# Kernel optimization log

Hardware: AMD Instinct MI355X
Metric: run time of the kernel (lower is better)

Reference implementation:

```python
import jax, jax.numpy as jnp
import numpy as np
import math

B, T, C = 2, 2048, 1024
H, D = 16, 64
GAMMA = 8

def setup_inputs() -> dict:
    key = jax.random.key(0)
    ks = jax.random.split(key, 6)
    s = 1.0 / math.sqrt(C)  # keep pre-softmax scores well-scaled
    return {
        "x": jax.random.normal(ks[0], (B, T, C), jnp.float32),
        "Wq": jax.random.normal(ks[1], (C, 2 * C), jnp.float32) * s,
        "Wk": jax.random.normal(ks[2], (C, 2 * C), jnp.float32) * s,
        "Wv": jax.random.normal(ks[3], (C, C), jnp.float32) * s,
        "Wo": jax.random.normal(ks[4], (C, C), jnp.float32) * s,
        "theta_offset": jax.random.normal(ks[5], (H,), jnp.float32) * 0.1,
    }

def _heads(t):  # (B,T,C) -> (B,H,T,D)
    return t.reshape(B, T, H, D).transpose(0, 2, 1, 3)

def reference(x, Wq, Wk, Wv, Wo, theta_offset):
    scale = 1.0 / math.sqrt(D)
    q_raw = x @ Wq            # (B,T,2C)
    k_raw = x @ Wk
    v = _heads(x @ Wv)        # (B,H,T,D)
    q_amp, q_phase = _heads(q_raw[..., :C]), _heads(q_raw[..., C:])
    k_amp, k_phase = _heads(k_raw[..., :C]), _heads(k_raw[..., C:])
    q_amp = jax.nn.softplus(q_amp)
    k_amp = jax.nn.softplus(k_amp)
    # sum_d a_q a_k cos(p_q - p_k) = (a_q cos p_q)(a_k cos p_k) + (a_q sin p_q)(a_k sin p_k)
    qc, qs = q_amp * jnp.cos(q_phase), q_amp * jnp.sin(q_phase)
    kc, ks_ = k_amp * jnp.cos(k_phase), k_amp * jnp.sin(k_phase)
    scores = (jnp.einsum('bhqd,bhkd->bhqk', qc, kc)
              + jnp.einsum('bhqd,bhkd->bhqk', qs, ks_)) * scale
    if T > GAMMA:  # theta gating
        cid = jnp.arange(T, dtype=jnp.float32) / GAMMA
        cycle_dist = cid[None, :] - cid[:, None]          # (T,T): cid[j]-cid[i]
        gate = jnp.cos(theta_offset[:, None, None] * cycle_dist[None])  # (H,T,T)
        scores = scores * gate[None]
    causal = jnp.tril(jnp.ones((T, T), dtype=bool))
    scores = jnp.where(causal[None, None], scores, -jnp.inf)
    attn = jax.nn.softmax(scores, axis=-1)
    out = jnp.einsum('bhqk,bhkd->bhqd', attn, v)
    out = out.transpose(0, 2, 1, 3).reshape(B, T, C)
    return out @ Wo
```

## Files before the change

### kernel.cpp

```cpp
#include <hip/hip_runtime.h>
#include <cmath>

namespace {

constexpr int B_ = 2, T_ = 2048, C_ = 1024, H_ = 16;
constexpr float GAMMA_INV = 0.125f;
constexpr float SCALE = 0.125f;
constexpr float LOG2E = 1.4426950408889634f;
constexpr float THR2 = 11.5415603f;

typedef __attribute__((ext_vector_type(8))) short bf16x8;
typedef __attribute__((ext_vector_type(4))) float f32x4;
typedef unsigned short ushort_t;

__device__ __forceinline__ ushort_t f2bf(float x) {
  union { float f; unsigned int u; } v; v.f = x;
  unsigned int r = (v.u + 0x7fffu + ((v.u >> 16) & 1u)) >> 16;
  return (ushort_t)r;
}

__device__ __forceinline__ unsigned pk_bf16(float a, float b) {
  unsigned r;
  asm("v_cvt_pk_bf16_f32 %0, %1, %2" : "=v"(r) : "v"(a), "v"(b));
  return r;
}

__device__ __forceinline__ float fexp2(float x) {
  return __builtin_amdgcn_exp2f(x);
}

__device__ __forceinline__ f32x4 mfma16(bf16x8 a, bf16x8 b, f32x4 c) {
  return __builtin_amdgcn_mfma_f32_16x16x32_bf16(a, b, c, 0, 0, 0);
}

__device__ __forceinline__ void gld_lds16(const ushort_t* g, ushort_t* l) {
  __builtin_amdgcn_global_load_lds(
      (const __attribute__((address_space(1))) unsigned int*)g,
      (__attribute__((address_space(3))) unsigned int*)l, 16, 0, 0);
}

constexpr int GBM = 128, GBN = 128, GBK = 64;

#define GEMM_CORE(A_, Bt_, K_)                                                  \
  __shared__ ushort_t As[GBM][GBK];                                             \
  __shared__ ushort_t Bs[GBN][GBK];                                             \
  const int tid = threadIdx.x;                                                  \
  const int wv = tid >> 6;                                                      \
  const int ln = tid & 63;                                                      \
  const int lr = ln & 15, hi = ln >> 4;                                         \
  const int wr = wv >> 1, wc = wv & 1;                                          \
  const int srow8 = tid >> 3;                                                   \
  const int ssw = ((tid & 7) ^ (srow8 & 7)) * 8;                                \
  const int kxg = (lr & 7) << 3;                                                \
  f32x4 acc[4][4];                                                              \
  _Pragma("unroll")                                                             \
  for (int m = 0; m < 4; ++m)                                                   \
    _Pragma("unroll")                                                           \
    for (int n = 0; n < 4; ++n)                                                 \
      _Pragma("unroll")                                                         \
      for (int r = 0; r < 4; ++r) acc[m][n][r] = 0.0f;                          \
  for (int k0 = 0; k0 < K_; k0 += GBK) {                                        \
    _Pragma("unroll")                                                           \
    for (int p = 0; p < 4; ++p) {                                               \
      gld_lds16(A_ + (size_t)(m0 + p * 32 + srow8) * K_ + k0 + ssw,             \
                &As[0][0] + p * 2048 + wv * 512);                               \
      gld_lds16(Bt_ + (size_t)(n0 + p * 32 + srow8) * K_ + k0 + ssw,            \
                &Bs[0][0] + p * 2048 + wv * 512);                               \
    }                                                                           \
    __syncthreads();                                                            \
    _Pragma("unroll")                                                           \
    for (int ks = 0; ks < 2; ++ks) {                                            \
      bf16x8 af[4], bfr[4];                                                     \
      _Pragma("unroll")                                                         \
      for (int m = 0; m < 4; ++m)                                               \
        af[m] = *(const bf16x8*)&As[wr * 64 + m * 16 + lr]                      \
                                  [(ks * 32 + hi * 8) ^ kxg];                   \
      _Pragma("unroll")                                                         \
      for (int n = 0; n < 4; ++n)                                               \
        bfr[n] = *(const bf16x8*)&Bs[wc * 64 + n * 16 + lr]                     \
                                   [(ks * 32 + hi * 8) ^ kxg];                  \
      _Pragma("unroll")                                                         \
      for (int m = 0; m < 4; ++m)                                               \
        _Pragma("unroll")                                                       \
        for (int n = 0; n < 4; ++n)                                             \
          acc[m][n] = mfma16(af[m], bfr[n], acc[m][n]);                         \
    }                                                                           \
    __syncthreads();                                                            \
  }

__global__ __launch_bounds__(256) void gemm_f32out(const ushort_t* __restrict__ A,
                                                   const ushort_t* __restrict__ Bt,
                                                   float* __restrict__ Cm,
                                                   int N, int K) {
  const int m0 = blockIdx.y * GBM, n0 = blockIdx.x * GBN;
  GEMM_CORE(A, Bt, K)
  #pragma unroll
  for (int m = 0; m < 4; ++m) {
    #pragma unroll
    for (int r = 0; r < 4; ++r) {
      const int row = m0 + wr * 64 + m * 16 + hi * 4 + r;
      float* Crow = Cm + (size_t)row * N + n0 + wc * 64;
      #pragma unroll
      for (int n = 0; n < 4; ++n)
        Crow[n * 16 + lr] = acc[m][n][r];
    }
  }
}

__global__ __launch_bounds__(256) void gemm_qkv(const ushort_t* __restrict__ A,
                                                const ushort_t* __restrict__ Bt,
                                                ushort_t* __restrict__ Qb,
                                                ushort_t* __restrict__ Kb,
                                                ushort_t* __restrict__ Vb,
                                                int K) {
  const int m0 = blockIdx.y * GBM, n0 = blockIdx.x * GBN;
  GEMM_CORE(A, Bt, K)
  if (n0 < 4096) {
    const int isK = (n0 >> 11) & 1;
    ushort_t* Dst = isK ? Kb : Qb;
    const int odd = lr & 1;
    #pragma unroll
    for (int m = 0; m < 4; ++m) {
      #pragma unroll
      for (int r = 0; r < 4; ++r) {
        const int row = m0 + wr * 64 + m * 16 + hi * 4 + r;
        #pragma unroll
        for (int n = 0; n < 4; ++n) {
          const int nn = n0 + wc * 64 + n * 16 + lr;
          float x = acc[m][n][r];
          float y = __shfl_xor(x, 1);
          float amp = odd ? y : x;
          float ph  = odd ? x : y;
          float sp = (amp > 20.f) ? amp : __logf(1.0f + __expf(amp));
          float val = sp * (odd ? __sinf(ph) : __cosf(ph));
          const int cc = (nn & 2047) >> 1;
          const int h = cc >> 6, d = cc & 63;
          const int t = row & (T_ - 1), b = row >> 11;
          Dst[(((size_t)(b * H_ + h) * T_) + t) * 128 + d + (odd ? 64 : 0)] = f2bf(val);
        }
      }
    }
  } else {
    const int v0 = n0 - 4096;
    #pragma unroll
    for (int m = 0; m < 4; ++m) {
      #pragma unroll
      for (int r = 0; r < 4; ++r) {
        const int row = m0 + wr * 64 + m * 16 + hi * 4 + r;
        ushort_t* Crow = Vb + (size_t)row * 1024 + v0 + wc * 64;
        #pragma unroll
        for (int n = 0; n < 4; ++n)
          Crow[n * 16 + lr] = f2bf(acc[m][n][r]);
      }
    }
  }
}

__global__ __launch_bounds__(256) void prep(const float* __restrict__ x,
                                            const float* __restrict__ Wq,
                                            const float* __restrict__ Wk,
                                            const float* __restrict__ Wv,
                                            const float* __restrict__ Wo,
                                            ushort_t* __restrict__ xb,
                                            ushort_t* __restrict__ Wqkt,
                                            ushort_t* __restrict__ Wvt,
                                            ushort_t* __restrict__ Wot) {
  __shared__ float tf[32][33];
  const int id = blockIdx.x;
  const int i = threadIdx.x;
  if (id < 4096) {
    const int e = (id * 256 + i) * 4;
    float4 a = *(const float4*)&x[e];
    uint2 p;
    p.x = (unsigned)f2bf(a.x) | ((unsigned)f2bf(a.y) << 16);
    p.y = (unsigned)f2bf(a.z) | ((unsigned)f2bf(a.w) << 16);
    *(uint2*)&xb[e] = p;
  } else if (id < 8192) {
    const int id2 = id - 4096;
    const int k0 = (id2 & 31) * 32, n0 = (id2 >> 5) * 32;
    const float* src = (n0 < 2048) ? Wq : Wk;
    const int c0 = (n0 & 2047) >> 1;
    {
      const int r = i >> 3, c4 = (i & 7) * 4;
      const int scol = (c4 < 16) ? (c0 + c4) : (1024 + c0 + c4 - 16);
      float4 v = *(const float4*)&src[(size_t)(k0 + r) * 2048 + scol];
      tf[r][c4 + 0] = v.x; tf[r][c4 + 1] = v.y; tf[r][c4 + 2] = v.z; tf[r][c4 + 3] = v.w;
    }
    __syncthreads();
    {
      const int orow = i >> 3, k4 = (i & 7) * 4;
      const int sel = (orow >> 1) + ((orow & 1) ? 16 : 0);
      uint2 p;
      p.x = (unsigned)f2bf(tf[k4 + 0][sel]) | ((unsigned)f2bf(tf[k4 + 1][sel]) << 16);
      p.y = (unsigned)f2bf(tf[k4 + 2][sel]) | ((unsigned)f2bf(tf[k4 + 3][sel]) << 16);
      *(uint2*)&Wqkt[(size_t)(n0 + orow) * 1024 + k0 + k4] = p;
    }
  } else {
    const int id3 = (id < 9216) ? (id - 8192) : (id - 9216);
    const float* W = (id < 9216) ? Wv : Wo;
    ushort_t* Wt = (id < 9216) ? Wvt : Wot;
    const int k0 = (id3 >> 5) * 32, n0 = (id3 & 31) * 32;
    {
      const int r = i >> 3, c4 = (i & 7) * 4;
      float4 v = *(const float4*)&W[(size_t)(k0 + r) * 1024 + n0 + c4];
      tf[r][c4 + 0] = v.x; tf[r][c4 + 1] = v.y; tf[r][c4 + 2] = v.z; tf[r][c4 + 3] = v.w;
    }
    __syncthreads();
    {
      const int r = i >> 3, c4 = (i & 7) * 4;
      uint2 p;
      p.x = (unsigned)f2bf(tf[c4 + 0][r]) | ((unsigned)f2bf(tf[c4 + 1][r]) << 16);
      p.y = (unsigned)f2bf(tf[c4 + 2][r]) | ((unsigned)f2bf(tf[c4 + 3][r]) << 16);
      *(uint2*)&Wt[(size_t)(n0 + r) * 1024 + k0 + c4] = p;
    }
  }
}

__global__ __launch_bounds__(256) void v_transpose(const ushort_t* __restrict__ V,
                                                   ushort_t* __restrict__ VT) {
  const int bh = blockIdx.y;
  const int b = bh >> 4, h = bh & 15;
  const int t0 = blockIdx.x * 32;
  __shared__ ushort_t lds[32][72];
  const int i = threadIdx.x;
  {
    int r = i >> 3, d0 = (i & 7) * 8;
    const ushort_t* src = V + ((size_t)(b * T_) + t0 + r) * C_ + h * 64 + d0;
    uint4 v = *(const uint4*)src;
    *(uint4*)&lds[r][d0] = v;
  }
  __syncthreads();
  {
    int d = i >> 2, tq = (i & 3) * 8;
    ushort_t tmp[8];
    #pragma unroll
    for (int j = 0; j < 8; ++j) tmp[j] = lds[tq + j][d];
    ulonglong2 pk;
    pk.x = (unsigned long long)tmp[0] | ((unsigned long long)tmp[1] << 16) |
           ((unsigned long long)tmp[2] << 32) | ((unsigned long long)tmp[3] << 48);
    pk.y = (unsigned long long)tmp[4] | ((unsigned long long)tmp[5] << 16) |
           ((unsigned long long)tmp[6] << 32) | ((unsigned long long)tmp[7] << 48);
    *(ulonglong2*)(VT + ((size_t)bh * 64 + d) * T_ + t0 + tq) = pk;
  }
}

__global__ __launch_bounds__(256) void attn_split(const ushort_t* __restrict__ Q,
                                                  const ushort_t* __restrict__ K,
                                                  const ushort_t* __restrict__ VT,
                                                  const float* __restrict__ theta,
                                                  unsigned* __restrict__ Op,
                                                  float* __restrict__ mpart,
                                                  float* __restrict__ lpart) {
  const int id = blockIdx.x;
  const int xcd = id & 7, sub = id >> 3;
  const int bhl = sub / 40;
  const int u = 39 - (sub - bhl * 40);
  int qt, s, ns;
  if (u < 4)       { qt = u;                 s = 0;             ns = 1; }
  else if (u < 12) { qt = 4 + ((u - 4) >> 1);  s = (u - 4) & 1;   ns = 2; }
  else if (u < 24) { qt = 8 + (u - 12) / 3;    s = (u - 12) % 3;  ns = 3; }
  else             { qt = 12 + ((u - 24) >> 2); s = (u - 24) & 3; ns = 4; }
  const int nktf = 2 * qt + 2;
  const int t0 = (s * nktf) / ns;
  const int t1 = ((s + 1) * nktf) / ns;
  const int bh = xcd * 4 + bhl;
  const int p = bh * 40 + u;
  unsigned* Op_my = Op + (size_t)p * 4096;

  const int h = bh & 15;
  const int tid = threadIdx.x;
  const int wid = tid >> 6, lane = tid & 63;
  const int q_base = qt * 128 + wid * 32;
  const int lr = lane & 15, lg = lane >> 4;
  const int kx = (lr & 7) << 4;

  __shared__ alignas(16) ushort_t Ksh[2][64 * 128];
  __shared__ alignas(16) ushort_t Vsh[64 * 64];

  const float th = theta[h];
  const int q_lo = q_base + lr;
  const int q_hi = q_base + 16 + lr;

  bf16x8 qfl[4], qfh[4];
  {
    const ushort_t* Qrow = Q + ((size_t)bh * T_ + q_lo) * 128 + lg * 8;
    #pragma unroll
    for (int ks = 0; ks < 4; ++ks) {
      qfl[ks] = *(const bf16x8*)(Qrow + ks * 32);
      qfh[ks] = *(const bf16x8*)(Qrow + 16 * 128 + ks * 32);
    }
  }

  const float cql = cosf(th * (float)q_lo * GAMMA_INV) * (SCALE * LOG2E);
  const float sql = sinf(th * (float)q_lo * GAMMA_INV) * (SCALE * LOG2E);
  const float cqh = cosf(th * (float)q_hi * GAMMA_INV) * (SCALE * LOG2E);
  const float sqh = sinf(th * (float)q_hi * GAMMA_INV) * (SCALE * LOG2E);
  float ck[4], sk[4];
  #pragma unroll
  for (int r = 0; r < 4; ++r) {
    float ang = th * (float)(t0 * 64 + lg * 4 + r) * GAMMA_INV;
    ck[r] = cosf(ang); sk[r] = sinf(ang);
  }
  float Ajl[4], Bjl[4], Ajh[4], Bjh[4];
  {
    const float c2 = cosf(th * 2.0f), s2 = sinf(th * 2.0f);
    float cj = 1.0f, sj = 0.0f;
    #pragma unroll
    for (int j = 0; j < 4; ++j) {
      Ajl[j] = cql * cj + sql * sj;
      Bjl[j] = sql * cj - cql * sj;
      Ajh[j] = cqh * cj + sqh * sj;
      Bjh[j] = sqh * cj - cqh * sj;
      float t0r = cj * c2 - sj * s2;
      sj = sj * c2 + cj * s2;
      cj = t0r;
    }
  }
  const float cd8 = cosf(th * 8.0f), sd8 = sinf(th * 8.0f);

  f32x4 o_lo[4], o_hi[4];
  #pragma unroll
  for (int n = 0; n < 4; ++n)
    #pragma unroll
    for (int r = 0; r < 4; ++r) { o_lo[n][r] = 0.0f; o_hi[n][r] = 0.0f; }
  float m_lo = -1e30f, l_lo = 0.0f, m_hi = -1e30f, l_hi = 0.0f;

  const ushort_t* Kbh = K + (size_t)bh * T_ * 128;
  const int srow = lane >> 4;
  const int scol = (lane & 15) * 8;
  const int vd = tid >> 2;
  const int vce = (tid & 3) * 16;
  const ushort_t* Vgb = VT + ((size_t)bh * 64 + vd) * T_ + vce;
  uint4 vreg[2];

  {
    const int k0 = t0 * 64;
    #pragma unroll
    for (int c = 0; c < 4; ++c) {
      const int r7 = 4 * (c & 1) + srow;
      const ushort_t* src = Kbh + (size_t)(k0 + 16 * wid + 4 * c + srow) * 128
                            + (scol ^ (r7 << 3));
      gld_lds16(src, &Ksh[0][(wid * 4 + c) * 512]);
    }
    #pragma unroll
    for (int c = 0; c < 2; ++c) vreg[c] = *(const uint4*)(Vgb + k0 + c * 8);
    #pragma unroll
    for (int c = 0; c < 2; ++c) {
      int byte = (vce * 2 + c * 16) ^ ((vd & 7) << 4);
      *(uint4*)&Vsh[vd * 64 + (byte >> 1)] = vreg[c];
    }
  }
  __syncthreads();

  for (int kt = t0; kt < t1; ++kt) {
    const int cur = (kt - t0) & 1;
    const int k0 = kt * 64;
    const bool more = (kt + 1) < t1;
    if (more) {
      const int kn = (kt + 1) * 64;
      #pragma unroll
      for (int c = 0; c < 4; ++c) {
        const int r7 = 4 * (c & 1) + srow;
        const ushort_t* src = Kbh + (size_t)(kn + 16 * wid + 4 * c + srow) * 128
                              + (scol ^ (r7 << 3));
        gld_lds16(src, &Ksh[cur ^ 1][(wid * 4 + c) * 512]);
      }
      #pragma unroll
      for (int c = 0; c < 2; ++c) vreg[c] = *(const uint4*)(Vgb + kn + c * 8);
    }
    f32x4 sl[4], sh[4];
    #pragma unroll
    for (int j = 0; j < 4; ++j)
      #pragma unroll
      for (int r = 0; r < 4; ++r) { sl[j][r] = 0.0f; sh[j][r] = 0.0f; }
    #pragma unroll
    for (int j = 0; j < 4; ++j) {
      const int rbase = (j * 16 + lr) * 128;
      #pragma unroll
      for (int ks = 0; ks < 4; ++ks) {
        const int byte = (ks * 64 + lg * 16) ^ kx;
        bf16x8 kf = *(const bf16x8*)&Ksh[cur][rbase + (byte >> 1)];
        sl[j] = mfma16(kf, qfl[ks], sl[j]);
        sh[j] = mfma16(kf, qfh[ks], sh[j]);
      }
    }
    float vl[4][4], vh[4][4];
    #pragma unroll
    for (int j = 0; j < 4; ++j)
      #pragma unroll
      for (int r = 0; r < 4; ++r) {
        const int kk = k0 + j * 16 + lg * 4 + r;
        float xl = sl[j][r] * (Ajl[j] * ck[r] + Bjl[j] * sk[r]);
        float xh = sh[j][r] * (Ajh[j] * ck[r] + Bjh[j] * sk[r]);
        vl[j][r] = (kk > q_lo) ? -3e30f : xl;
        vh[j][r] = (kk > q_hi) ? -3e30f : xh;
      }
    float tml = vl[0][0], tmh = vh[0][0];
    #pragma unroll
    for (int j = 0; j < 4; ++j)
      #pragma unroll
      for (int r = 0; r < 4; ++r) { tml = fmaxf(tml, vl[j][r]); tmh = fmaxf(tmh, vh[j][r]); }
    tml = fmaxf(tml, __shfl_xor(tml, 16));
    tml = fmaxf(tml, __shfl_xor(tml, 32));
    tmh = fmaxf(tmh, __shfl_xor(tmh, 16));
    tmh = fmaxf(tmh, __shfl_xor(tmh, 32));
    if (__ballot(tml > m_lo + THR2 || tmh > m_hi + THR2)) {
      float mnl = fmaxf(m_lo, tml), mnh = fmaxf(m_hi, tmh);
      float el = fexp2(m_lo - mnl), eh = fexp2(m_hi - mnh);
      m_lo = mnl; m_hi = mnh;
      l_lo *= el; l_hi *= eh;
      #pragma unroll
      for (int r = 0; r < 4; ++r) {
        float erl = __shfl(el, lg * 4 + r);
        float erh = __shfl(eh, lg * 4 + r);
        #pragma unroll
        for (int n = 0; n < 4; ++n) { o_lo[n][r] *= erl; o_hi[n][r] *= erh; }
      }
    }
    float el[4][4], eh[4][4], psl = 0.0f, psh = 0.0f;
    #pragma unroll
    for (int j = 0; j < 4; ++j)
      #pragma unroll
      for (int r = 0; r < 4; ++r) {
        el[j][r] = fexp2(vl[j][r] - m_lo);
        eh[j][r] = fexp2(vh[j][r] - m_hi);
        psl += el[j][r];
        psh += eh[j][r];
      }
    psl += __shfl_xor(psl, 16);
    psl += __shfl_xor(psl, 32);
    psh += __shfl_xor(psh, 16);
    psh += __shfl_xor(psh, 32);
    l_lo += psl; l_hi += psh;
    bf16x8 pal[2], pah[2];
    #pragma unroll
    for (int hh = 0; hh < 2; ++hh) {
      union { bf16x8 v8; unsigned u4[4]; } ul, uh;
      ul.u4[0] = pk_bf16(el[2 * hh][0], el[2 * hh][1]);
      ul.u4[1] = pk_bf16(el[2 * hh][2], el[2 * hh][3]);
      ul.u4[2] = pk_bf16(el[2 * hh + 1][0], el[2 * hh + 1][1]);
      ul.u4[3] = pk_bf16(el[2 * hh + 1][2], el[2 * hh + 1][3]);
      uh.u4[0] = pk_bf16(eh[2 * hh][0], eh[2 * hh][1]);
      uh.u4[1] = pk_bf16(eh[2 * hh][2], eh[2 * hh][3]);
      uh.u4[2] = pk_bf16(eh[2 * hh + 1][0], eh[2 * hh + 1][1]);
      uh.u4[3] = pk_bf16(eh[2 * hh + 1][2], eh[2 * hh + 1][3]);
      pal[hh] = ul.v8; pah[hh] = uh.v8;
    }
    #pragma unroll
    for (int n = 0; n < 4; ++n) {
      const int dbase = (n * 16 + lr) * 64;
      #pragma unroll
      for (int hh = 0; hh < 2; ++hh) {
        const int b0 = (hh * 64 + lg * 8) ^ kx;
        const int b1 = (hh * 64 + 32 + lg * 8) ^ kx;
        union { bf16x8 v8; uint2 u2[2]; } uu;
        uu.u2[0] = *(const uint2*)&Vsh[dbase + (b0 >> 1)];
        uu.u2[1] = *(const uint2*)&Vsh[dbase + (b1 >> 1)];
        o_lo[n] = mfma16(pal[hh], uu.v8, o_lo[n]);
        o_hi[n] = mfma16(pah[hh], uu.v8, o_hi[n]);
      }
    }
    #pragma unroll
    for (int r = 0; r < 4; ++r) {
      float t0r = ck[r] * cd8 - sk[r] * sd8;
      sk[r] = sk[r] * cd8 + ck[r] * sd8;
      ck[r] = t0r;
    }
    __syncthreads();
    if (more) {
      #pragma unroll
      for (int c = 0; c < 2; ++c) {
        int byte = (vce * 2 + c * 16) ^ ((vd & 7) << 4);
        *(uint4*)&Vsh[vd * 64 + (byte >> 1)] = vreg[c];
      }
      __syncthreads();
    }
  }
  #pragma unroll
  for (int r = 0; r < 4; ++r) {
    const int pr = wid * 16 + lg * 4 + r;
    #pragma unroll
    for (int n = 0; n < 4; ++n) {
      Op_my[pr * 64 + n * 16 + lr] =
          (unsigned)f2bf(o_lo[n][r]) | ((unsigned)f2bf(o_hi[n][r]) << 16);
    }
  }
  if (lg == 0) {
    mpart[p * 128 + wid * 32 + lr] = m_lo;
    lpart[p * 128 + wid * 32 + lr] = l_lo;
    mpart[p * 128 + wid * 32 + 16 + lr] = m_hi;
    lpart[p * 128 + wid * 32 + 16 + lr] = l_hi;
  }
}

__global__ __launch_bounds__(256) void attn_comb(const unsigned* __restrict__ Op,
                                                 const float* __restrict__ mpart,
                                                 const float* __restrict__ lpart,
                                                 ushort_t* __restrict__ O) {
  const int id = blockIdx.x;
  const int bh = id >> 4, qt = id & 15;
  const int b = bh >> 4, h = bh & 15;
  int base, ns;
  if (qt < 4)       { base = qt;                 ns = 1; }
  else if (qt < 8)  { base = 4 + 2 * (qt - 4);   ns = 2; }
  else if (qt < 12) { base = 12 + 3 * (qt - 8);  ns = 3; }
  else              { base = 24 + 4 * (qt - 12); ns = 4; }
  const int tid = threadIdx.x;
  const int r = tid >> 1, d0 = (tid & 1) * 32;
  const int pr = ((r >> 5) << 4) + (r & 15);
  const int hi = (r >> 4) & 1;

  float ms[4], ls[4];
  float M = -3e30f;
  for (int s2 = 0; s2 < ns; ++s2) {
    const int p = bh * 40 + base + s2;
    ms[s2] = mpart[p * 128 + r];
    ls[s2] = lpart[p * 128 + r];
    M = fmaxf(M, ms[s2]);
  }
  float acc[32];
  #pragma unroll
  for (int i = 0; i < 32; ++i) acc[i] = 0.0f;
  float denom = 0.0f;
  for (int s2 = 0; s2 < ns; ++s2) {
    const int p = bh * 40 + base + s2;
    const float w = fexp2(ms[s2] - M);
    denom += w * ls[s2];
    const unsigned* a = Op + (size_t)p * 4096 + pr * 64 + d0;
    #pragma unroll
    for (int c = 0; c < 8; ++c) {
      uint4 v = *(const uint4*)(a + c * 4);
      const unsigned uu[4] = {v.x, v.y, v.z, v.w};
      #pragma unroll
      for (int q2 = 0; q2 < 4; ++q2) {
        union { unsigned u; float f; } cv;
        cv.u = hi ? (uu[q2] & 0xFFFF0000u) : (uu[q2] << 16);
        acc[c * 4 + q2] += w * cv.f;
      }
    }
  }
  const float inv = 1.0f / denom;
  unsigned po[16];
  #pragma unroll
  for (int i = 0; i < 16; ++i)
    po[i] = (unsigned)f2bf(acc[2 * i] * inv) | ((unsigned)f2bf(acc[2 * i + 1] * inv) << 16);
  const int q = qt * 128 + r;
  ushort_t* dst = O + ((size_t)b * T_ + q) * C_ + h * 64 + d0;
  *(uint4*)(dst + 0)  = make_uint4(po[0], po[1], po[2], po[3]);
  *(uint4*)(dst + 8)  = make_uint4(po[4], po[5], po[6], po[7]);
  *(uint4*)(dst + 16) = make_uint4(po[8], po[9], po[10], po[11]);
  *(uint4*)(dst + 24) = make_uint4(po[12], po[13], po[14], po[15]);
}

}

extern "C" void kernel_launch(void* const* d_in, const int* in_sizes, int n_in,
                              void* d_out, int out_size, void* d_ws, size_t ws_size,
                              hipStream_t stream) {
  const float* x  = (const float*)d_in[0];
  const float* Wq = (const float*)d_in[1];
  const float* Wk = (const float*)d_in[2];
  const float* Wv = (const float*)d_in[3];
  const float* Wo = (const float*)d_in[4];
  const float* th = (const float*)d_in[5];
  float* out = (float*)d_out;
  float* ws = (float*)d_ws;

  unsigned* Op    = (unsigned*)ws;
  ushort_t* Vb    = (ushort_t*)ws;
  ushort_t* xb    = (ushort_t*)(ws + 4194304);
  ushort_t* Wqkvt = (ushort_t*)(ws + 6291456);
  ushort_t* Wvt   = Wqkvt + (size_t)4096 * 1024;
  ushort_t* Qb    = (ushort_t*)(ws + 10485760);
  ushort_t* Ob    = (ushort_t*)(ws + 10485760);
  ushort_t* Kb    = (ushort_t*)(ws + 14680064);
  ushort_t* vt    = (ushort_t*)(ws + 18874368);
  float* mpart    = ws + 20971520;
  float* lpart    = ws + 21135360;
  ushort_t* Wot   = (ushort_t*)(ws + 21495808);

  dim3 blk(256);
  prep<<<10240, blk, 0, stream>>>(x, Wq, Wk, Wv, Wo, xb, Wqkvt, Wvt, Wot);
  gemm_qkv<<<dim3(40, 32), blk, 0, stream>>>(xb, Wqkvt, Qb, Kb, Vb, 1024);
  v_transpose<<<dim3(64, 32), blk, 0, stream>>>(Vb, vt);
  attn_split<<<1280, blk, 0, stream>>>(Qb, Kb, vt, th, Op, mpart, lpart);
  attn_comb<<<512, blk, 0, stream>>>(Op, mpart, lpart, Ob);
  gemm_f32out<<<dim3(8, 32), blk, 0, stream>>>(Ob, Wot, out, 1024, 1024);
}
```

Measured before the change: 191.4 us.

## Double-buffer GEMM LDS tiles to overlap global loads with MFMA compute

The shared GEMM core gets ping-pong LDS buffers for the A and B tiles. The next K-tile is prefetched with global_load_lds before the current tile is computed, and a partial vmcnt wait replaces the full __syncthreads. This is meant to hide global-to-LDS latency behind the MFMA work. It doubles LDS use to 64KB per block, which may lower occupancy. It also relies on hand-written waitcnt and barrier ordering being correct.

```diff
diff --git a/kernel.cpp b/kernel.cpp
--- a/kernel.cpp
+++ b/kernel.cpp
@@ -42,8 +42,8 @@
 constexpr int GBM = 128, GBN = 128, GBK = 64;
 
 #define GEMM_CORE(A_, Bt_, K_)                                                  \
-  __shared__ ushort_t As[GBM][GBK];                                             \
-  __shared__ ushort_t Bs[GBN][GBK];                                             \
+  __shared__ ushort_t As[2][GBM][GBK];                                          \
+  __shared__ ushort_t Bs[2][GBM][GBK];                                          \
   const int tid = threadIdx.x;                                                  \
   const int wv = tid >> 6;                                                      \
   const int ln = tid & 63;                                                      \
@@ -59,25 +59,40 @@
     for (int n = 0; n < 4; ++n)                                                 \
       _Pragma("unroll")                                                         \
       for (int r = 0; r < 4; ++r) acc[m][n][r] = 0.0f;                          \
+                                                 \
+  _Pragma("unroll")                                                             \
+  for (int p = 0; p < 4; ++p) {                                                 \
+    gld_lds16(A_ + (size_t)(m0 + p * 32 + srow8) * K_ + ssw,                    \
+              &As[0][0][0] + p * 2048 + wv * 512);                              \
+    gld_lds16(Bt_ + (size_t)(n0 + p * 32 + srow8) * K_ + ssw,                   \
+              &Bs[0][0][0] + p * 2048 + wv * 512);                              \
+  }                                                                             \
   for (int k0 = 0; k0 < K_; k0 += GBK) {                                        \
-    _Pragma("unroll")                                                           \
-    for (int p = 0; p < 4; ++p) {                                               \
-      gld_lds16(A_ + (size_t)(m0 + p * 32 + srow8) * K_ + k0 + ssw,             \
-                &As[0][0] + p * 2048 + wv * 512);                               \
-      gld_lds16(Bt_ + (size_t)(n0 + p * 32 + srow8) * K_ + k0 + ssw,            \
-                &Bs[0][0] + p * 2048 + wv * 512);                               \
+    const int cur = (k0 >> 6) & 1;                                              \
+    const bool more = (k0 + GBK) < K_;                                          \
+    if (more) {                                                                 \
+      _Pragma("unroll")                                                         \
+      for (int p = 0; p < 4; ++p) {                                             \
+        gld_lds16(A_ + (size_t)(m0 + p * 32 + srow8) * K_ + k0 + GBK + ssw,     \
+                  &As[cur ^ 1][0][0] + p * 2048 + wv * 512);                    \
+        gld_lds16(Bt_ + (size_t)(n0 + p * 32 + srow8) * K_ + k0 + GBK + ssw,    \
+                  &Bs[cur ^ 1][0][0] + p * 2048 + wv * 512);                    \
+      }                                                                         \
+      asm volatile("s_waitcnt vmcnt(8)" ::: "memory");                          \
+    } else {                                                                    \
+      asm volatile("s_waitcnt vmcnt(0)" ::: "memory");                          \
     }                                                                           \
-    __syncthreads();                                                            \
+    __builtin_amdgcn_s_barrier();                                               \
     _Pragma("unroll")                                                           \
     for (int ks = 0; ks < 2; ++ks) {                                            \
       bf16x8 af[4], bfr[4];                                                     \
       _Pragma("unroll")                                                         \
       for (int m = 0; m < 4; ++m)                                               \
-        af[m] = *(const bf16x8*)&As[wr * 64 + m * 16 + lr]                      \
+        af[m] = *(const bf16x8*)&As[cur][wr * 64 + m * 16 + lr]                 \
                                   [(ks * 32 + hi * 8) ^ kxg];                   \
       _Pragma("unroll")                                                         \
       for (int n = 0; n < 4; ++n)                                               \
-        bfr[n] = *(const bf16x8*)&Bs[wc * 64 + n * 16 + lr]                     \
+        bfr[n] = *(const bf16x8*)&Bs[cur][wc * 64 + n * 16 + lr]                \
                                    [(ks * 32 + hi * 8) ^ kxg];                  \
       _Pragma("unroll")                                                         \
       for (int m = 0; m < 4; ++m)                                               \
@@ -85,7 +100,7 @@
         for (int n = 0; n < 4; ++n)                                             \
           acc[m][n] = mfma16(af[m], bfr[n], acc[m][n]);                         \
     }                                                                           \
-    __syncthreads();                                                            \
+    __builtin_amdgcn_s_barrier();                                               \
   }
 
 __global__ __launch_bounds__(256) void gemm_f32out(const ushort_t* __restrict__ A,
```

Result: no change. 190.0 us (-0.8%).
